# Kernel optimization log

Measured on AMD Instinct MI355X. Metric: run time of the kernel, lower is better.

Reference implementation:

```python
import jax, jax.numpy as jnp
import numpy as np

DIM = 512
DEPTH = 6
HEADS = 8
HD = DIM // HEADS          # head dim = 64
HALF = HD // 4             # rope half_dim = 16
MLP_H = int(DIM * 4.0)
TOKENS = [1, 4, 16, 64]    # CLS, S1, S2, S3
N = sum(TOKENS)            # 85
MAX_FREQ = 10.0
BATCH = 1024
LN_EPS = 1e-5


def _build_mask():
    # CLS sees CLS+S3; each scale sees CLS+itself (block-diagonal + CLS column)
    m = np.full((N, N), -np.inf, dtype=np.float32)
    cum = np.cumsum([0] + TOKENS)  # [0,1,5,21,85]
    m[0, 0] = 0.0
    m[0, cum[3]:cum[4]] = 0.0
    for i in range(1, 4):
        s, e = cum[i], cum[i + 1]
        m[s:e, 0] = 0.0
        m[s:e, s:e] = 0.0
    return jnp.asarray(m)

MASK = _build_mask()
FREQS = jnp.exp(jnp.arange(HALF, dtype=jnp.float32) * (-np.log(MAX_FREQ) / HALF))


def _layer_norm(x, g, b):
    mu = x.mean(-1, keepdims=True)
    var = ((x - mu) ** 2).mean(-1, keepdims=True)
    return (x - mu) * jax.lax.rsqrt(var + LN_EPS) * g + b


def _rope2d(t, coords):
    # t: [B,H,P,HD], coords: [P,2] in [0,1]^2
    ang_x = coords[:, 0:1] * FREQS[None, :] * (2.0 * jnp.pi)  # [P,HALF]
    ang_y = coords[:, 1:2] * FREQS[None, :] * (2.0 * jnp.pi)
    cx, sx = jnp.cos(ang_x), jnp.sin(ang_x)
    cy, sy = jnp.cos(ang_y), jnp.sin(ang_y)
    B, H, P, _ = t.shape
    t = t.reshape(B, H, P, 4, HALF)
    x0, x1, x2, x3 = t[..., 0, :], t[..., 1, :], t[..., 2, :], t[..., 3, :]
    r = jnp.stack([x0 * cx - x1 * sx,
                   x0 * sx + x1 * cx,
                   x2 * cy - x3 * sy,
                   x2 * sy + x3 * cy], axis=3)
    return r.reshape(B, H, P, HD)


def _rope_skip_cls(t, coords):
    return jnp.concatenate([t[:, :, :1], _rope2d(t[:, :, 1:], coords)], axis=2)


def _block(x, coords, p):
    (ln1g, ln1b, qkvw, qkvb, projw, projb,
     ln2g, ln2b, f1w, f1b, f2w, f2b) = p
    B, Nn, D = x.shape
    h = _layer_norm(x, ln1g, ln1b)
    qkv = h @ qkvw + qkvb                         # [B,N,3D]
    qkv = qkv.reshape(B, Nn, 3, HEADS, HD).transpose(2, 0, 3, 1, 4)
    q, k, v = qkv[0], qkv[1], qkv[2]              # [B,H,N,HD]
    q = _rope_skip_cls(q, coords)
    k = _rope_skip_cls(k, coords)
    attn = jnp.einsum('bhqd,bhkd->bhqk', q, k) * (HD ** -0.5) + MASK
    attn = jax.nn.softmax(attn, axis=-1)
    out = jnp.einsum('bhqk,bhkd->bhqd', attn, v)
    out = out.transpose(0, 2, 1, 3).reshape(B, Nn, D)
    x = x + (out @ projw + projb)
    h = _layer_norm(x, ln2g, ln2b)
    h = jax.nn.gelu(h @ f1w + f1b, approximate=False) @ f2w + f2b
    return x + h


def setup_inputs() -> dict:
    key = jax.random.key(0)
    ks = jax.random.split(key, 8)
    s = 0.02
    nrm = lambda k, shape: jax.random.normal(k, shape, jnp.float32) * s
    return dict(
        x=jax.random.normal(ks[0], (BATCH, N, DIM), jnp.float32),
        coords=jax.random.uniform(ks[1], (N - 1, 2), jnp.float32),
        ln1_g=jnp.ones((DEPTH, DIM), jnp.float32),
        ln1_b=jnp.zeros((DEPTH, DIM), jnp.float32),
        qkv_w=nrm(ks[2], (DEPTH, DIM, 3 * DIM)),
        qkv_b=jnp.zeros((DEPTH, 3 * DIM), jnp.float32),
        proj_w=nrm(ks[3], (DEPTH, DIM, DIM)),
        proj_b=jnp.zeros((DEPTH, DIM), jnp.float32),
        ln2_g=jnp.ones((DEPTH, DIM), jnp.float32),
        ln2_b=jnp.zeros((DEPTH, DIM), jnp.float32),
        fc1_w=nrm(ks[4], (DEPTH, DIM, MLP_H)),
        fc1_b=jnp.zeros((DEPTH, MLP_H), jnp.float32),
        fc2_w=nrm(ks[5], (DEPTH, MLP_H, DIM)),
        fc2_b=jnp.zeros((DEPTH, DIM), jnp.float32),
    )


def reference(x, coords, ln1_g, ln1_b, qkv_w, qkv_b, proj_w, proj_b,
              ln2_g, ln2_b, fc1_w, fc1_b, fc2_w, fc2_b):
    for i in range(DEPTH):
        x = _block(x, coords,
                   (ln1_g[i], ln1_b[i], qkv_w[i], qkv_b[i], proj_w[i], proj_b[i],
                    ln2_g[i], ln2_b[i], fc1_w[i], fc1_b[i], fc2_w[i], fc2_b[i]))
    return x
```

## Files before the change

### kernel.cpp

```cpp
#include <hip/hip_runtime.h>
#include <hip/hip_bf16.h>
#include <math.h>

#define DIMX 512
#define NTOK 85
#define BATCH 1024
#define M_ROWS (BATCH * NTOK)
#define MLP_H 2048
#define DEPTH 6

typedef __attribute__((ext_vector_type(8))) short short8;
typedef __attribute__((ext_vector_type(4))) float f32x4;

__device__ inline float bf2f(ushort u) {
    union { unsigned int i; float f; } v; v.i = ((unsigned int)u) << 16; return v.f;
}
__device__ inline ushort f2bf(float f) {
    __hip_bfloat16 h = __float2bfloat16(f);
    union { __hip_bfloat16 h; ushort u; } v; v.h = h; return v.u;
}
__device__ inline unsigned int pack2(float a, float b) {
    return (unsigned int)f2bf(a) | ((unsigned int)f2bf(b) << 16);
}

__device__ inline void gload16(const ushort* g, ushort* lds) {
    __builtin_amdgcn_global_load_lds(
        (const __attribute__((address_space(1))) unsigned int*)g,
        (__attribute__((address_space(3))) unsigned int*)lds, 16, 0, 0);
}

__global__ __launch_bounds__(256) void transpose_bf16(const float* __restrict__ in,
                                                      ushort* __restrict__ out,
                                                      int K, int N) {
    __shared__ float tile[32][33];
    int n0 = blockIdx.x * 32, k0 = blockIdx.y * 32;
    int tx = threadIdx.x, ty = threadIdx.y;
    #pragma unroll
    for (int j = 0; j < 32; j += 8)
        tile[ty + j][tx] = in[(size_t)(k0 + ty + j) * N + n0 + tx];
    __syncthreads();
    #pragma unroll
    for (int j = 0; j < 32; j += 8)
        out[(size_t)(n0 + ty + j) * K + k0 + tx] = f2bf(tile[tx][ty + j]);
}

__global__ void rope_table(const float* __restrict__ coords, float* __restrict__ tab) {
    int t = blockIdx.x;
    int idx = threadIdx.x;
    float freq = expf(-(float)idx * (2.302585093f / 16.0f));
    float twopi = 6.283185307179586f;
    float ax = coords[t * 2 + 0] * freq * twopi;
    float ay = coords[t * 2 + 1] * freq * twopi;
    tab[t * 64 + idx]      = cosf(ax);
    tab[t * 64 + 16 + idx] = sinf(ax);
    tab[t * 64 + 32 + idx] = cosf(ay);
    tab[t * 64 + 48 + idx] = sinf(ay);
}

__global__ __launch_bounds__(256) void ln_kernel(const float* __restrict__ x,
                                                 const float* __restrict__ g,
                                                 const float* __restrict__ bta,
                                                 ushort* __restrict__ out) {
    int w = threadIdx.x >> 6, lane = threadIdx.x & 63;
    size_t row = (size_t)blockIdx.x * 4 + w;
    const float* xr = x + row * DIMX;
    int c = lane * 8;
    float4 v0 = *(const float4*)(xr + c);
    float4 v1 = *(const float4*)(xr + c + 4);
    float s = v0.x + v0.y + v0.z + v0.w + v1.x + v1.y + v1.z + v1.w;
    #pragma unroll
    for (int m = 32; m; m >>= 1) s += __shfl_xor(s, m);
    float mu = s * (1.0f / 512.0f);
    float d0 = v0.x - mu, d1 = v0.y - mu, d2 = v0.z - mu, d3 = v0.w - mu;
    float d4 = v1.x - mu, d5 = v1.y - mu, d6 = v1.z - mu, d7 = v1.w - mu;
    float q = d0*d0 + d1*d1 + d2*d2 + d3*d3 + d4*d4 + d5*d5 + d6*d6 + d7*d7;
    #pragma unroll
    for (int m = 32; m; m >>= 1) q += __shfl_xor(q, m);
    float rs = rsqrtf(q * (1.0f / 512.0f) + 1e-5f);
    float4 g0 = *(const float4*)(g + c), g1 = *(const float4*)(g + c + 4);
    float4 b0 = *(const float4*)(bta + c), b1 = *(const float4*)(bta + c + 4);
    uint4 o;
    o.x = pack2(d0 * rs * g0.x + b0.x, d1 * rs * g0.y + b0.y);
    o.y = pack2(d2 * rs * g0.z + b0.z, d3 * rs * g0.w + b0.w);
    o.z = pack2(d4 * rs * g1.x + b1.x, d5 * rs * g1.y + b1.y);
    o.w = pack2(d6 * rs * g1.z + b1.z, d7 * rs * g1.w + b1.w);
    *(uint4*)&out[row * DIMX + c] = o;
}

template <int EPI>
__global__ __launch_bounds__(512, 2) void gemm_bt(const ushort* __restrict__ A,
                                                  const ushort* __restrict__ Bt,
                                                  const float* __restrict__ bias,
                                                  float* __restrict__ outF,
                                                  ushort* __restrict__ outB,
                                                  int M, int N, int K,
                                                  const float* __restrict__ tab) {
    __shared__ ushort As[4][256 * 32] __attribute__((aligned(16)));
    __shared__ ushort Bs[4][256 * 32] __attribute__((aligned(16)));
    int tid = threadIdx.x;
    int w = tid >> 6, lane = tid & 63;
    int wm2 = (w >> 2) * 128;
    int wn4 = (w & 3) * 64;

    int nbx = gridDim.x;
    int nwg = nbx * gridDim.y;
    int orig = blockIdx.y * nbx + blockIdx.x;
    int q8 = nwg >> 3, r8 = nwg & 7;
    int xcd = orig & 7, loc = orig >> 3;
    int id = (xcd < r8) ? xcd * (q8 + 1) + loc : r8 * (q8 + 1) + (xcd - r8) * q8 + loc;
    int m0 = (id / nbx) * 256;
    int n0 = (id % nbx) * 256;

    int g1i = tid + 512;
    int r0 = tid >> 2, r1 = g1i >> 2;
    int q0 = (tid & 3) ^ ((r0 >> 1) & 3);
    int q1 = (g1i & 3) ^ ((r1 >> 1) & 3);
    int ar0 = m0 + r0; if (ar0 >= M) ar0 = M - 1;
    int ar1 = m0 + r1; if (ar1 >= M) ar1 = M - 1;
    const ushort* apA0 = A + (size_t)ar0 * K + q0 * 8;
    const ushort* apA1 = A + (size_t)ar1 * K + q1 * 8;
    const ushort* bpB0 = Bt + (size_t)(n0 + r0) * K + q0 * 8;
    const ushort* bpB1 = Bt + (size_t)(n0 + r1) * K + q1 * 8;
    int d0 = w * 512;
    int d1 = w * 512 + 4096;

    int l15 = lane & 15, lq = lane >> 4;
    int sw = (lq ^ ((l15 >> 1) & 3)) * 8;
    int aoff = (wm2 + l15) * 32 + sw;
    int boff = (wn4 + l15) * 32 + sw;

    int NT = K >> 5;

#define STAGE(T) do { int kc = (T) * 32, sl = (T) & 3;                      \
        gload16(apA0 + kc, &As[sl][d0]); gload16(apA1 + kc, &As[sl][d1]);   \
        gload16(bpB0 + kc, &Bs[sl][d0]); gload16(bpB1 + kc, &Bs[sl][d1]); } while (0)

    STAGE(0); STAGE(1); STAGE(2);

    f32x4 acc[8][4] = {};

    for (int t = 0; t < NT; ++t) {
        if (t < NT - 2)       asm volatile("s_waitcnt vmcnt(8)" ::: "memory");
        else if (t == NT - 2) asm volatile("s_waitcnt vmcnt(4)" ::: "memory");
        else                  asm volatile("s_waitcnt vmcnt(0)" ::: "memory");
        __builtin_amdgcn_s_barrier();
        const ushort* sa = As[t & 3];
        const ushort* sb = Bs[t & 3];
        short8 a[8], b[4];
        #pragma unroll
        for (int i = 0; i < 8; i++) a[i] = *(const short8*)&sa[aoff + i * 512];
        #pragma unroll
        for (int j = 0; j < 4; j++) b[j] = *(const short8*)&sb[boff + j * 512];
        if (t + 3 < NT) STAGE(t + 3);
        asm volatile("s_waitcnt lgkmcnt(0)" ::: "memory");
        __builtin_amdgcn_sched_barrier(0);
        __builtin_amdgcn_s_setprio(1);
        #pragma unroll
        for (int i = 0; i < 8; i++)
            #pragma unroll
            for (int j = 0; j < 4; j++)
                acc[i][j] = __builtin_amdgcn_mfma_f32_16x16x32_bf16(a[i], b[j], acc[i][j], 0, 0, 0);
        __builtin_amdgcn_s_setprio(0);
    }
#undef STAGE

    int cr = lq * 4;
    int cc = l15;
    if (EPI == 0) {
        bool ropeReg = (n0 + wn4) < 1024;
        int gnb = n0 + wn4 + cc;
        float bb0 = bias[gnb], bb1 = bias[gnb + 16], bb2 = bias[gnb + 32], bb3 = bias[gnb + 48];
        #pragma unroll
        for (int i = 0; i < 8; i++) {
            #pragma unroll
            for (int rr = 0; rr < 4; rr++) {
                int gm = m0 + wm2 + i * 16 + cr + rr;
                if (gm >= M) continue;
                int n = gm % NTOK;
                float v0 = acc[i][0][rr] + bb0;
                float v1 = acc[i][1][rr] + bb1;
                float v2 = acc[i][2][rr] + bb2;
                float v3 = acc[i][3][rr] + bb3;
                if (ropeReg && n > 0) {
                    const float* tt = tab + (size_t)(n - 1) * 64 + cc;
                    float cx = tt[0], sx = tt[16], cy = tt[32], sy = tt[48];
                    float y0 = v0 * cx - v1 * sx;
                    float y1 = v0 * sx + v1 * cx;
                    float y2 = v2 * cy - v3 * sy;
                    float y3 = v2 * sy + v3 * cy;
                    v0 = y0; v1 = y1; v2 = y2; v3 = y3;
                }
                size_t o = (size_t)gm * N + gnb;
                outB[o]      = f2bf(v0);
                outB[o + 16] = f2bf(v1);
                outB[o + 32] = f2bf(v2);
                outB[o + 48] = f2bf(v3);
            }
        }
    } else {
        #pragma unroll
        for (int i = 0; i < 8; i++) {
            #pragma unroll
            for (int rr = 0; rr < 4; rr++) {
                int gm = m0 + wm2 + i * 16 + cr + rr;
                if (gm >= M) continue;
                #pragma unroll
                for (int j = 0; j < 4; j++) {
                    int gn = n0 + wn4 + j * 16 + cc;
                    float v = acc[i][j][rr] + bias[gn];
                    size_t o = (size_t)gm * N + gn;
                    if (EPI == 1) {
                        outF[o] = outF[o] + v;
                    } else {
                        float ge = 0.5f * v * (1.0f + erff(v * 0.70710678118f));
                        outB[o] = f2bf(ge);
                    }
                }
            }
        }
    }
}

__global__ __launch_bounds__(384) void attn_kernel(const ushort* __restrict__ qkv,
                                                   ushort* __restrict__ out) {
    __shared__ ushort SU[13824] __attribute__((aligned(16)));
    __shared__ ushort Vt[6656]  __attribute__((aligned(16)));
    int bh = blockIdx.x;
    int b = bh >> 3, h = bh & 7;
    int tid = threadIdx.x;
    size_t base = (size_t)b * NTOK * 1536 + h * 64;

    for (int it = tid; it < 1536; it += 384) {
        int mat = (it >= 768) ? 1 : 0;
        int item = it - mat * 768;
        int n = item >> 3, g = item & 7;
        short8 v = {};
        if (n < NTOK)
            v = *(const short8*)&qkv[base + (size_t)n * 1536 + mat * 512 + g * 8];
        *(short8*)&SU[mat * 6912 + n * 72 + g * 8] = v;
    }
    for (int it = tid; it < 768; it += 384) {
        int n = it % 96;
        int d0 = (it / 96) * 8;
        short8 v = {};
        if (n < NTOK)
            v = *(const short8*)&qkv[base + (size_t)n * 1536 + 1024 + d0];
        #pragma unroll
        for (int j = 0; j < 8; j++)
            Vt[(d0 + j) * 104 + n] = (ushort)v[j];
    }
    __syncthreads();

    int wid = tid >> 6;
    int lane = tid & 63;
    int q = lane >> 4, c = lane & 15;
    int i0 = wid * 16;

    f32x4 acc[6] = {};
    #pragma unroll
    for (int kk = 0; kk < 2; kk++) {
        short8 aq = *(const short8*)&SU[(i0 + c) * 72 + kk * 32 + q * 8];
        #pragma unroll
        for (int t = 0; t < 6; t++) {
            short8 bk = *(const short8*)&SU[6912 + (t * 16 + c) * 72 + kk * 32 + q * 8];
            acc[t] = __builtin_amdgcn_mfma_f32_16x16x32_bf16(aq, bk, acc[t], 0, 0, 0);
        }
    }
    __syncthreads();

    #pragma unroll
    for (int r = 0; r < 4; r++) {
        int i = i0 + q * 4 + r;
        int si = (i == 0) ? 3 : (i < 5 ? 1 : (i < 21 ? 2 : 3));
        float vs[6];
        float m = -1e30f;
        #pragma unroll
        for (int t = 0; t < 6; t++) {
            int j = t * 16 + c;
            int sj = (j == 0) ? si : (j < 5 ? 1 : (j < 21 ? 2 : (j < NTOK ? 3 : -1)));
            float v = (sj == si) ? acc[t][r] * 0.125f : -1e30f;
            vs[t] = v;
            m = fmaxf(m, v);
        }
        #pragma unroll
        for (int mk = 8; mk; mk >>= 1) m = fmaxf(m, __shfl_xor(m, mk));
        float s = 0.f, ps[6];
        #pragma unroll
        for (int t = 0; t < 6; t++) { ps[t] = __expf(vs[t] - m); s += ps[t]; }
        #pragma unroll
        for (int mk = 8; mk; mk >>= 1) s += __shfl_xor(s, mk);
        float inv = 1.0f / s;
        #pragma unroll
        for (int t = 0; t < 6; t++)
            SU[i * 104 + t * 16 + c] = f2bf(ps[t] * inv);
    }
    __syncthreads();

    f32x4 o2[4] = {};
    #pragma unroll
    for (int kk = 0; kk < 3; kk++) {
        short8 ap = *(const short8*)&SU[(i0 + c) * 104 + kk * 32 + q * 8];
        #pragma unroll
        for (int nt = 0; nt < 4; nt++) {
            short8 bv = *(const short8*)&Vt[(nt * 16 + c) * 104 + kk * 32 + q * 8];
            o2[nt] = __builtin_amdgcn_mfma_f32_16x16x32_bf16(ap, bv, o2[nt], 0, 0, 0);
        }
    }
    size_t orow = (size_t)b * NTOK;
    #pragma unroll
    for (int nt = 0; nt < 4; nt++) {
        #pragma unroll
        for (int r = 0; r < 4; r++) {
            int i = i0 + q * 4 + r;
            if (i < NTOK)
                out[(orow + i) * DIMX + h * 64 + nt * 16 + c] = f2bf(o2[nt][r]);
        }
    }
}

extern "C" void kernel_launch(void* const* d_in, const int* in_sizes, int n_in,
                              void* d_out, int out_size, void* d_ws, size_t ws_size,
                              hipStream_t stream) {
    const float* x_in    = (const float*)d_in[0];
    const float* coords  = (const float*)d_in[1];
    const float* ln1_g   = (const float*)d_in[2];
    const float* ln1_b   = (const float*)d_in[3];
    const float* qkv_w   = (const float*)d_in[4];
    const float* qkv_b   = (const float*)d_in[5];
    const float* proj_w  = (const float*)d_in[6];
    const float* proj_b  = (const float*)d_in[7];
    const float* ln2_g   = (const float*)d_in[8];
    const float* ln2_b   = (const float*)d_in[9];
    const float* fc1_w   = (const float*)d_in[10];
    const float* fc1_b   = (const float*)d_in[11];
    const float* fc2_w   = (const float*)d_in[12];
    const float* fc2_b   = (const float*)d_in[13];

    char* ws = (char*)d_ws;
    size_t off = 0;
    auto alloc = [&](size_t bytes) -> void* {
        void* p = ws + off;
        off += (bytes + 255) & ~(size_t)255;
        return p;
    };
    auto asz = [](size_t b) { return (b + 255) & ~(size_t)255; };

    const size_t WPL = 512 * 1536 + 512 * 512 + 512 * 2048 + 2048 * 512;

    size_t fixed = asz(WPL * DEPTH * sizeof(ushort)) + asz(84 * 64 * sizeof(float));
    int Bc = 1024;
    while (Bc > 4) {
        size_t rc = (size_t)Bc * NTOK;
        size_t need = fixed + asz(rc * DIMX * sizeof(ushort)) + asz(rc * MLP_H * sizeof(ushort));
        if (need <= ws_size) break;
        Bc >>= 1;
    }
    size_t Rc = (size_t)Bc * NTOK;

    ushort* wt   = (ushort*)alloc(WPL * DEPTH * sizeof(ushort));
    float*  tab  = (float*)alloc(84 * 64 * sizeof(float));
    ushort* hbuf = (ushort*)alloc(Rc * DIMX * sizeof(ushort));
    ushort* big  = (ushort*)alloc(Rc * MLP_H * sizeof(ushort));

    hipMemcpyAsync(d_out, x_in, (size_t)M_ROWS * DIMX * sizeof(float),
                   hipMemcpyDeviceToDevice, stream);

    rope_table<<<84, 16, 0, stream>>>(coords, tab);

    dim3 tb(32, 8);
    for (int l = 0; l < DEPTH; l++) {
        ushort* wl = wt + (size_t)l * WPL;
        transpose_bf16<<<dim3(1536 / 32, 512 / 32), tb, 0, stream>>>(
            qkv_w + (size_t)l * 512 * 1536, wl, 512, 1536);
        transpose_bf16<<<dim3(512 / 32, 512 / 32), tb, 0, stream>>>(
            proj_w + (size_t)l * 512 * 512, wl + 786432, 512, 512);
        transpose_bf16<<<dim3(2048 / 32, 512 / 32), tb, 0, stream>>>(
            fc1_w + (size_t)l * 512 * 2048, wl + 1048576, 512, 2048);
        transpose_bf16<<<dim3(512 / 32, 2048 / 32), tb, 0, stream>>>(
            fc2_w + (size_t)l * 2048 * 512, wl + 2097152, 2048, 512);
    }

    int mt = (int)((Rc + 255) / 256);
    int lnblocks = (int)(Rc / 4);
    for (int c = 0; c < BATCH / Bc; c++) {
        float* xc = (float*)d_out + (size_t)c * Rc * DIMX;
        int Mc = (int)Rc;
        for (int l = 0; l < DEPTH; l++) {
            ushort* wl = wt + (size_t)l * WPL;
            ln_kernel<<<lnblocks, 256, 0, stream>>>(
                xc, ln1_g + l * 512, ln1_b + l * 512, hbuf);
            gemm_bt<0><<<dim3(1536 / 256, mt), 512, 0, stream>>>(
                hbuf, wl, qkv_b + (size_t)l * 1536, nullptr, big, Mc, 1536, 512, tab);
            attn_kernel<<<Bc * 8, 384, 0, stream>>>(big, hbuf);
            gemm_bt<1><<<dim3(512 / 256, mt), 512, 0, stream>>>(
                hbuf, wl + 786432, proj_b + (size_t)l * 512, xc, nullptr,
                Mc, 512, 512, nullptr);
            ln_kernel<<<lnblocks, 256, 0, stream>>>(
                xc, ln2_g + l * 512, ln2_b + l * 512, hbuf);
            gemm_bt<2><<<dim3(2048 / 256, mt), 512, 0, stream>>>(
                hbuf, wl + 1048576, fc1_b + (size_t)l * 2048, nullptr, big,
                Mc, 2048, 512, nullptr);
            gemm_bt<1><<<dim3(512 / 256, mt), 512, 0, stream>>>(
                big, wl + 2097152, fc2_b + (size_t)l * 512, xc, nullptr,
                Mc, 512, 2048, nullptr);
        }
    }
}
```

Before: 7.841 ms.

## Restructure GEMM main loop into 64-wide K steps with split half-tile MFMA phases

Replaces the 4-slot, 32-wide K pipeline in the bf16 GEMM with a double-buffered 64-wide K step, where each step has two 32-wide halves. Each half runs as two MFMA phases, and global-to-LDS loads for the next halves are issued between them. This spreads the async loads across the compute to improve overlap and to cut register pressure for A fragments (4 instead of 8 live). The cost is more barriers and waitcnt points, and a more intricate vmcnt accounting that could stall or race if miscounted.

New measurement: 7.697 ms. About the same (-1.8%).

```diff
diff --git a/kernel.cpp b/kernel.cpp
--- a/kernel.cpp
+++ b/kernel.cpp
@@ -95,8 +95,8 @@
                                                   ushort* __restrict__ outB,
                                                   int M, int N, int K,
                                                   const float* __restrict__ tab) {
-    __shared__ ushort As[4][256 * 32] __attribute__((aligned(16)));
-    __shared__ ushort Bs[4][256 * 32] __attribute__((aligned(16)));
+    __shared__ ushort As[2][2][8192] __attribute__((aligned(16)));
+    __shared__ ushort Bs[2][2][8192] __attribute__((aligned(16)));
     int tid = threadIdx.x;
     int w = tid >> 6, lane = tid & 63;
     int wm2 = (w >> 2) * 128;
@@ -111,58 +111,115 @@
     int m0 = (id / nbx) * 256;
     int n0 = (id % nbx) * 256;
 
-    int g1i = tid + 512;
-    int r0 = tid >> 2, r1 = g1i >> 2;
-    int q0 = (tid & 3) ^ ((r0 >> 1) & 3);
-    int q1 = (g1i & 3) ^ ((r1 >> 1) & 3);
-    int ar0 = m0 + r0; if (ar0 >= M) ar0 = M - 1;
-    int ar1 = m0 + r1; if (ar1 >= M) ar1 = M - 1;
-    const ushort* apA0 = A + (size_t)ar0 * K + q0 * 8;
-    const ushort* apA1 = A + (size_t)ar1 * K + q1 * 8;
-    const ushort* bpB0 = Bt + (size_t)(n0 + r0) * K + q0 * 8;
-    const ushort* bpB1 = Bt + (size_t)(n0 + r1) * K + q1 * 8;
-    int d0 = w * 512;
-    int d1 = w * 512 + 4096;
+    int srow = tid >> 2;
+    int schunk = (tid & 3) ^ ((srow >> 1) & 3);
+    int arA0 = m0 + srow;       if (arA0 >= M) arA0 = M - 1;
+    int arA1 = m0 + 128 + srow; if (arA1 >= M) arA1 = M - 1;
+    const ushort* gA0 = A  + (size_t)arA0 * K + schunk * 8;
+    const ushort* gA1 = A  + (size_t)arA1 * K + schunk * 8;
+    const ushort* gB0 = Bt + (size_t)(n0 + srow) * K + schunk * 8;
+    const ushort* gB1 = Bt + (size_t)(n0 + 128 + srow) * K + schunk * 8;
+    int dst = w * 512;
+
+#define STA(J, KH) do { int kc = (J) * 64 + (KH) * 32; int bi = (J) & 1;      \
+        gload16(gA0 + kc, &As[bi][KH][dst]);                                  \
+        gload16(gA1 + kc, &As[bi][KH][4096 + dst]); } while (0)
+#define STB(J, KH) do { int kc = (J) * 64 + (KH) * 32; int bi = (J) & 1;      \
+        gload16(gB0 + kc, &Bs[bi][KH][dst]);                                  \
+        gload16(gB1 + kc, &Bs[bi][KH][4096 + dst]); } while (0)
 
     int l15 = lane & 15, lq = lane >> 4;
     int sw = (lq ^ ((l15 >> 1) & 3)) * 8;
     int aoff = (wm2 + l15) * 32 + sw;
     int boff = (wn4 + l15) * 32 + sw;
 
-    int NT = K >> 5;
-
-#define STAGE(T) do { int kc = (T) * 32, sl = (T) & 3;                      \
-        gload16(apA0 + kc, &As[sl][d0]); gload16(apA1 + kc, &As[sl][d1]);   \
-        gload16(bpB0 + kc, &Bs[sl][d0]); gload16(bpB1 + kc, &Bs[sl][d1]); } while (0)
-
-    STAGE(0); STAGE(1); STAGE(2);
+    int NT = K >> 6;
+
+    STA(0, 0); STB(0, 0);
+    STA(0, 1); STB(0, 1);
+    STA(1, 0); STB(1, 0);
 
     f32x4 acc[8][4] = {};
 
-    for (int t = 0; t < NT; ++t) {
-        if (t < NT - 2)       asm volatile("s_waitcnt vmcnt(8)" ::: "memory");
-        else if (t == NT - 2) asm volatile("s_waitcnt vmcnt(4)" ::: "memory");
-        else                  asm volatile("s_waitcnt vmcnt(0)" ::: "memory");
+    for (int j = 0; j < NT; ++j) {
+        int bi = j & 1;
+        bool more1 = (j + 1 < NT);
+        bool more2 = (j + 2 < NT);
+        const ushort* saL = &As[bi][0][0];
+        const ushort* sbL = &Bs[bi][0][0];
+        const ushort* saH = &As[bi][1][0];
+        const ushort* sbH = &Bs[bi][1][0];
+
+        if (more1) asm volatile("s_waitcnt vmcnt(8)" ::: "memory");
+        else       asm volatile("s_waitcnt vmcnt(4)" ::: "memory");
         __builtin_amdgcn_s_barrier();
-        const ushort* sa = As[t & 3];
-        const ushort* sb = Bs[t & 3];
-        short8 a[8], b[4];
-        #pragma unroll
-        for (int i = 0; i < 8; i++) a[i] = *(const short8*)&sa[aoff + i * 512];
-        #pragma unroll
-        for (int j = 0; j < 4; j++) b[j] = *(const short8*)&sb[boff + j * 512];
-        if (t + 3 < NT) STAGE(t + 3);
-        asm volatile("s_waitcnt lgkmcnt(0)" ::: "memory");
-        __builtin_amdgcn_sched_barrier(0);
-        __builtin_amdgcn_s_setprio(1);
-        #pragma unroll
-        for (int i = 0; i < 8; i++)
-            #pragma unroll
-            for (int j = 0; j < 4; j++)
-                acc[i][j] = __builtin_amdgcn_mfma_f32_16x16x32_bf16(a[i], b[j], acc[i][j], 0, 0, 0);
-        __builtin_amdgcn_s_setprio(0);
-    }
-#undef STAGE
+        {
+            short8 a[4], b[4];
+            #pragma unroll
+            for (int i = 0; i < 4; i++) a[i] = *(const short8*)&saL[aoff + i * 512];
+            #pragma unroll
+            for (int jb = 0; jb < 4; jb++) b[jb] = *(const short8*)&sbL[boff + jb * 512];
+            if (more1) STA(j + 1, 1);
+            asm volatile("s_waitcnt lgkmcnt(0)" ::: "memory");
+            __builtin_amdgcn_sched_barrier(0);
+            __builtin_amdgcn_s_setprio(1);
+            #pragma unroll
+            for (int i = 0; i < 4; i++)
+                #pragma unroll
+                for (int jb = 0; jb < 4; jb++)
+                    acc[i][jb] = __builtin_amdgcn_mfma_f32_16x16x32_bf16(a[i], b[jb], acc[i][jb], 0, 0, 0);
+            __builtin_amdgcn_s_setprio(0);
+            short8 a2[4];
+            #pragma unroll
+            for (int i = 0; i < 4; i++) a2[i] = *(const short8*)&saL[aoff + (i + 4) * 512];
+            if (more1) STB(j + 1, 1);
+            asm volatile("s_waitcnt lgkmcnt(0)" ::: "memory");
+            __builtin_amdgcn_sched_barrier(0);
+            __builtin_amdgcn_s_setprio(1);
+            #pragma unroll
+            for (int i = 0; i < 4; i++)
+                #pragma unroll
+                for (int jb = 0; jb < 4; jb++)
+                    acc[i + 4][jb] = __builtin_amdgcn_mfma_f32_16x16x32_bf16(a2[i], b[jb], acc[i + 4][jb], 0, 0, 0);
+            __builtin_amdgcn_s_setprio(0);
+        }
+
+        if (more1) asm volatile("s_waitcnt vmcnt(8)" ::: "memory");
+        else       asm volatile("s_waitcnt vmcnt(0)" ::: "memory");
+        __builtin_amdgcn_s_barrier();
+        {
+            short8 a[4], b[4];
+            #pragma unroll
+            for (int i = 0; i < 4; i++) a[i] = *(const short8*)&saH[aoff + i * 512];
+            #pragma unroll
+            for (int jb = 0; jb < 4; jb++) b[jb] = *(const short8*)&sbH[boff + jb * 512];
+            if (more2) STA(j + 2, 0);
+            asm volatile("s_waitcnt lgkmcnt(0)" ::: "memory");
+            __builtin_amdgcn_sched_barrier(0);
+            __builtin_amdgcn_s_setprio(1);
+            #pragma unroll
+            for (int i = 0; i < 4; i++)
+                #pragma unroll
+                for (int jb = 0; jb < 4; jb++)
+                    acc[i][jb] = __builtin_amdgcn_mfma_f32_16x16x32_bf16(a[i], b[jb], acc[i][jb], 0, 0, 0);
+            __builtin_amdgcn_s_setprio(0);
+            short8 a2[4];
+            #pragma unroll
+            for (int i = 0; i < 4; i++) a2[i] = *(const short8*)&saH[aoff + (i + 4) * 512];
+            if (more2) STB(j + 2, 0);
+            asm volatile("s_waitcnt lgkmcnt(0)" ::: "memory");
+            __builtin_amdgcn_sched_barrier(0);
+            __builtin_amdgcn_s_setprio(1);
+            #pragma unroll
+            for (int i = 0; i < 4; i++)
+                #pragma unroll
+                for (int jb = 0; jb < 4; jb++)
+                    acc[i + 4][jb] = __builtin_amdgcn_mfma_f32_16x16x32_bf16(a2[i], b[jb], acc[i + 4][jb], 0, 0, 0);
+            __builtin_amdgcn_s_setprio(0);
+        }
+    }
+#undef STA
+#undef STB
 
     int cr = lq * 4;
     int cc = l15;
```

## Switch GEMMs to 256x128 double-buffered tiles and use tanh-form GELU

Applied to the files above, without the earlier changes.

Replaces the 512-thread 256x256 GEMM, which had a 4-stage LDS pipeline, with a 256-thread 256x128 kernel. The new kernel double-buffers LDS and adds an extra barrier before issuing the next stage's loads. The aim is to lower LDS use per block and improve occupancy and grid balance. The fc1 epilogue now uses a sigmoid-based tanh GELU approximation instead of erff, to cut transcendental cost. Two risks: the row-tile count now rounds down, which assumes the chunk rows are a multiple of 256, and the GELU output differs slightly from the exact erf form.

After: 7.220 ms. 7.9% less time.

```diff
diff --git a/kernel.cpp b/kernel.cpp
--- a/kernel.cpp
+++ b/kernel.cpp
@@ -21,6 +21,10 @@
 }
 __device__ inline unsigned int pack2(float a, float b) {
     return (unsigned int)f2bf(a) | ((unsigned int)f2bf(b) << 16);
+}
+__device__ inline float gelu_fast(float v) {
+    float u = 1.5957691f * fmaf(0.044715f * v, v * v, v);
+    return v / (1.0f + __expf(-u));
 }
 
 __device__ inline void gload16(const ushort* g, ushort* lds) {
@@ -88,19 +92,19 @@
 }
 
 template <int EPI>
-__global__ __launch_bounds__(512, 2) void gemm_bt(const ushort* __restrict__ A,
-                                                  const ushort* __restrict__ Bt,
-                                                  const float* __restrict__ bias,
-                                                  float* __restrict__ outF,
-                                                  ushort* __restrict__ outB,
-                                                  int M, int N, int K,
-                                                  const float* __restrict__ tab) {
-    __shared__ ushort As[4][256 * 32] __attribute__((aligned(16)));
-    __shared__ ushort Bs[4][256 * 32] __attribute__((aligned(16)));
+__global__ __launch_bounds__(256, 2) void gemm_wide(const ushort* __restrict__ A,
+                                                    const ushort* __restrict__ Bt,
+                                                    const float* __restrict__ bias,
+                                                    float* __restrict__ outF,
+                                                    ushort* __restrict__ outB,
+                                                    int M, int N, int K,
+                                                    const float* __restrict__ tab) {
+    __shared__ ushort As[2][256 * 32] __attribute__((aligned(16)));
+    __shared__ ushort Bs[2][128 * 32] __attribute__((aligned(16)));
     int tid = threadIdx.x;
     int w = tid >> 6, lane = tid & 63;
-    int wm2 = (w >> 2) * 128;
-    int wn4 = (w & 3) * 64;
+    int wm2 = (w >> 1) * 128;
+    int wn = (w & 1) * 64;
 
     int nbx = gridDim.x;
     int nwg = nbx * gridDim.y;
@@ -109,50 +113,56 @@
     int xcd = orig & 7, loc = orig >> 3;
     int id = (xcd < r8) ? xcd * (q8 + 1) + loc : r8 * (q8 + 1) + (xcd - r8) * q8 + loc;
     int m0 = (id / nbx) * 256;
-    int n0 = (id % nbx) * 256;
-
-    int g1i = tid + 512;
-    int r0 = tid >> 2, r1 = g1i >> 2;
-    int q0 = (tid & 3) ^ ((r0 >> 1) & 3);
-    int q1 = (g1i & 3) ^ ((r1 >> 1) & 3);
-    int ar0 = m0 + r0; if (ar0 >= M) ar0 = M - 1;
-    int ar1 = m0 + r1; if (ar1 >= M) ar1 = M - 1;
-    const ushort* apA0 = A + (size_t)ar0 * K + q0 * 8;
-    const ushort* apA1 = A + (size_t)ar1 * K + q1 * 8;
-    const ushort* bpB0 = Bt + (size_t)(n0 + r0) * K + q0 * 8;
-    const ushort* bpB1 = Bt + (size_t)(n0 + r1) * K + q1 * 8;
-    int d0 = w * 512;
-    int d1 = w * 512 + 4096;
+    int n0 = (id % nbx) * 128;
+
+    int srow = tid >> 2;
+    int scol = ((tid & 3) ^ ((srow >> 1) & 3)) * 8;
+    const ushort* gAp[4];
+    const ushort* gBp[2];
+    #pragma unroll
+    for (int rn = 0; rn < 4; rn++) {
+        int rr2 = m0 + srow + rn * 64; if (rr2 >= M) rr2 = M - 1;
+        gAp[rn] = A + (size_t)rr2 * K + scol;
+    }
+    #pragma unroll
+    for (int rn = 0; rn < 2; rn++)
+        gBp[rn] = Bt + (size_t)(n0 + srow + rn * 64) * K + scol;
+    int dwz = w * 512;
+
+#define STAGEW(T) do { int kc = (T) * 32, sl = (T) & 1;                        \
+        gload16(gAp[0] + kc, &As[sl][dwz]);                                    \
+        gload16(gAp[1] + kc, &As[sl][2048 + dwz]);                             \
+        gload16(gAp[2] + kc, &As[sl][4096 + dwz]);                             \
+        gload16(gAp[3] + kc, &As[sl][6144 + dwz]);                             \
+        gload16(gBp[0] + kc, &Bs[sl][dwz]);                                    \
+        gload16(gBp[1] + kc, &Bs[sl][2048 + dwz]); } while (0)
 
     int l15 = lane & 15, lq = lane >> 4;
     int sw = (lq ^ ((l15 >> 1) & 3)) * 8;
     int aoff = (wm2 + l15) * 32 + sw;
-    int boff = (wn4 + l15) * 32 + sw;
+    int boff = (wn + l15) * 32 + sw;
 
     int NT = K >> 5;
 
-#define STAGE(T) do { int kc = (T) * 32, sl = (T) & 3;                      \
-        gload16(apA0 + kc, &As[sl][d0]); gload16(apA1 + kc, &As[sl][d1]);   \
-        gload16(bpB0 + kc, &Bs[sl][d0]); gload16(bpB1 + kc, &Bs[sl][d1]); } while (0)
-
-    STAGE(0); STAGE(1); STAGE(2);
+    STAGEW(0); STAGEW(1);
 
     f32x4 acc[8][4] = {};
 
     for (int t = 0; t < NT; ++t) {
-        if (t < NT - 2)       asm volatile("s_waitcnt vmcnt(8)" ::: "memory");
-        else if (t == NT - 2) asm volatile("s_waitcnt vmcnt(4)" ::: "memory");
-        else                  asm volatile("s_waitcnt vmcnt(0)" ::: "memory");
+        if (t == NT - 1) asm volatile("s_waitcnt vmcnt(0)" ::: "memory");
+        else             asm volatile("s_waitcnt vmcnt(6)" ::: "memory");
         __builtin_amdgcn_s_barrier();
-        const ushort* sa = As[t & 3];
-        const ushort* sb = Bs[t & 3];
+        const ushort* sa = As[t & 1];
+        const ushort* sb = Bs[t & 1];
         short8 a[8], b[4];
         #pragma unroll
         for (int i = 0; i < 8; i++) a[i] = *(const short8*)&sa[aoff + i * 512];
         #pragma unroll
         for (int j = 0; j < 4; j++) b[j] = *(const short8*)&sb[boff + j * 512];
-        if (t + 3 < NT) STAGE(t + 3);
         asm volatile("s_waitcnt lgkmcnt(0)" ::: "memory");
+        __builtin_amdgcn_sched_barrier(0);
+        __builtin_amdgcn_s_barrier();
+        if (t + 2 < NT) STAGEW(t + 2);
         __builtin_amdgcn_sched_barrier(0);
         __builtin_amdgcn_s_setprio(1);
         #pragma unroll
@@ -162,13 +172,13 @@
                 acc[i][j] = __builtin_amdgcn_mfma_f32_16x16x32_bf16(a[i], b[j], acc[i][j], 0, 0, 0);
         __builtin_amdgcn_s_setprio(0);
     }
-#undef STAGE
+#undef STAGEW
 
     int cr = lq * 4;
     int cc = l15;
     if (EPI == 0) {
-        bool ropeReg = (n0 + wn4) < 1024;
-        int gnb = n0 + wn4 + cc;
+        bool ropeReg = (n0 + wn) < 1024;
+        int gnb = n0 + wn + cc;
         float bb0 = bias[gnb], bb1 = bias[gnb + 16], bb2 = bias[gnb + 32], bb3 = bias[gnb + 48];
         #pragma unroll
         for (int i = 0; i < 8; i++) {
@@ -206,14 +216,13 @@
                 if (gm >= M) continue;
                 #pragma unroll
                 for (int j = 0; j < 4; j++) {
-                    int gn = n0 + wn4 + j * 16 + cc;
+                    int gn = n0 + wn + j * 16 + cc;
                     float v = acc[i][j][rr] + bias[gn];
                     size_t o = (size_t)gm * N + gn;
                     if (EPI == 1) {
                         outF[o] = outF[o] + v;
                     } else {
-                        float ge = 0.5f * v * (1.0f + erff(v * 0.70710678118f));
-                        outB[o] = f2bf(ge);
+                        outB[o] = f2bf(gelu_fast(v));
                     }
                 }
             }
@@ -380,7 +389,7 @@
             fc2_w + (size_t)l * 2048 * 512, wl + 2097152, 2048, 512);
     }
 
-    int mt = (int)((Rc + 255) / 256);
+    int mt256 = (int)(Rc / 256);
     int lnblocks = (int)(Rc / 4);
     for (int c = 0; c < BATCH / Bc; c++) {
         float* xc = (float*)d_out + (size_t)c * Rc * DIMX;
@@ -389,18 +398,18 @@
             ushort* wl = wt + (size_t)l * WPL;
             ln_kernel<<<lnblocks, 256, 0, stream>>>(
                 xc, ln1_g + l * 512, ln1_b + l * 512, hbuf);
-            gemm_bt<0><<<dim3(1536 / 256, mt), 512, 0, stream>>>(
+            gemm_wide<0><<<dim3(1536 / 128, mt256), 256, 0, stream>>>(
                 hbuf, wl, qkv_b + (size_t)l * 1536, nullptr, big, Mc, 1536, 512, tab);
             attn_kernel<<<Bc * 8, 384, 0, stream>>>(big, hbuf);
-            gemm_bt<1><<<dim3(512 / 256, mt), 512, 0, stream>>>(
+            gemm_wide<1><<<dim3(512 / 128, mt256), 256, 0, stream>>>(
                 hbuf, wl + 786432, proj_b + (size_t)l * 512, xc, nullptr,
                 Mc, 512, 512, nullptr);
             ln_kernel<<<lnblocks, 256, 0, stream>>>(
                 xc, ln2_g + l * 512, ln2_b + l * 512, hbuf);
-            gemm_bt<2><<<dim3(2048 / 256, mt), 512, 0, stream>>>(
+            gemm_wide<2><<<dim3(2048 / 128, mt256), 256, 0, stream>>>(
                 hbuf, wl + 1048576, fc1_b + (size_t)l * 2048, nullptr, big,
                 Mc, 2048, 512, nullptr);
-            gemm_bt<1><<<dim3(512 / 256, mt), 512, 0, stream>>>(
+            gemm_wide<1><<<dim3(512 / 128, mt256), 256, 0, stream>>>(
                 big, wl + 2097152, fc2_b + (size_t)l * 512, xc, nullptr,
                 Mc, 512, 2048, nullptr);
         }
```
